# Kernel optimization log

Hardware: AMD Instinct MI355X
Metric: run time of the kernel (lower is better)

## Reference

```python
import jax, jax.numpy as jnp
import numpy as np
from jax import lax

D_MODEL, D_STATE, D_CONV, EXPAND = 192, 16, 3, 2
D_INNER = EXPAND * D_MODEL          # 384
DT_RANK = -(-D_MODEL // 16)         # 12
LN_EPS = 1e-5


def setup_inputs() -> dict:
    key = jax.random.key(0)
    ks = jax.random.split(key, 12)
    B, H, W = 4, 64, 64
    inv_sq = lambda n: 1.0 / np.sqrt(n)
    x = jax.random.normal(ks[0], (B, H, W, D_MODEL), jnp.float32)
    prompt = jax.random.normal(ks[1], (B, H, W, D_MODEL), jnp.float32)
    W_in = jax.random.normal(ks[2], (D_MODEL, 2 * D_INNER), jnp.float32) * inv_sq(D_MODEL)
    conv_w = jax.random.normal(ks[3], (D_INNER, 1, D_CONV, D_CONV), jnp.float32) * inv_sq(D_CONV * D_CONV)
    conv_b = jax.random.normal(ks[4], (D_INNER,), jnp.float32) * 0.02
    Wx = jax.random.normal(ks[5], (D_INNER, DT_RANK + 2 * D_STATE), jnp.float32) * inv_sq(D_INNER)
    Wdt = jax.random.uniform(ks[6], (DT_RANK, D_INNER), jnp.float32, -DT_RANK ** -0.5, DT_RANK ** -0.5)
    # dt bias init: inverse softplus of dt ~ LogUniform(1e-3, 0.1)
    dt = jnp.exp(jax.random.uniform(ks[7], (D_INNER,), jnp.float32) * (np.log(0.1) - np.log(1e-3)) + np.log(1e-3))
    dt = jnp.clip(dt, 1e-4, None)
    b_dt = dt + jnp.log(-jnp.expm1(-dt))
    A_log = jnp.log(jnp.broadcast_to(jnp.arange(1, D_STATE + 1, dtype=jnp.float32), (D_INNER, D_STATE)))
    D = jnp.ones((D_INNER,), jnp.float32)
    Wp = jax.random.normal(ks[8], (D_MODEL, D_STATE), jnp.float32) * inv_sq(D_MODEL)
    ln_g = jnp.ones((D_INNER,), jnp.float32)
    ln_b = jnp.zeros((D_INNER,), jnp.float32)
    Wout = jax.random.normal(ks[9], (D_INNER, D_MODEL), jnp.float32) * inv_sq(D_INNER)
    return dict(x=x, prompt=prompt, W_in=W_in, conv_w=conv_w, conv_b=conv_b, Wx=Wx,
                Wdt=Wdt, b_dt=b_dt, A_log=A_log, D=D, Wp=Wp, ln_g=ln_g, ln_b=ln_b, Wout=Wout)


def _selective_scan(u, delta, A, Bs, Cs, D):
    # u, delta: [B, L, d]; Bs, Cs: [B, L, n]; A: [d, n]; D: [d]
    Bsz = u.shape[0]
    h0 = jnp.zeros((Bsz, D_INNER, D_STATE), u.dtype)

    def step(h, inp):
        dl, uu, b, c = inp                      # [B,d],[B,d],[B,n],[B,n]
        dA = jnp.exp(dl[..., None] * A)          # [B,d,n]
        h = dA * h + (dl * uu)[..., None] * b[:, None, :]
        y = jnp.einsum('bdn,bn->bd', h, c)
        return h, y

    xs = (jnp.moveaxis(delta, 1, 0), jnp.moveaxis(u, 1, 0),
          jnp.moveaxis(Bs, 1, 0), jnp.moveaxis(Cs, 1, 0))
    _, ys = lax.scan(step, h0, xs)               # ys: [L,B,d]
    return jnp.moveaxis(ys, 0, 1) + u * D        # [B,L,d]


def reference(x, prompt, W_in, conv_w, conv_b, Wx, Wdt, b_dt, A_log, D, Wp, ln_g, ln_b, Wout):
    B, H, W, C = x.shape
    L = H * W
    xz = x @ W_in                                 # [B,H,W,2*d_inner]
    xi, z = jnp.split(xz, 2, axis=-1)
    # depthwise conv2d (NCHW, groups=d_inner)
    xc = jnp.transpose(xi, (0, 3, 1, 2))
    pad = (D_CONV - 1) // 2
    xc = lax.conv_general_dilated(xc, conv_w, (1, 1), [(pad, pad), (pad, pad)],
                                  dimension_numbers=('NCHW', 'OIHW', 'NCHW'),
                                  feature_group_count=D_INNER)
    xc = xc + conv_b[None, :, None, None]
    xc = jax.nn.silu(xc)
    u = jnp.transpose(xc.reshape(B, D_INNER, L), (0, 2, 1))   # [B,L,d]
    x_dbl = u @ Wx                                            # [B,L,r+2n]
    dtr = x_dbl[..., :DT_RANK]
    Bs = x_dbl[..., DT_RANK:DT_RANK + D_STATE]
    Cs = x_dbl[..., DT_RANK + D_STATE:]
    delta = jax.nn.softplus(dtr @ Wdt + b_dt)                 # [B,L,d] (delta_bias + softplus)
    Cs = Cs + prompt.reshape(B, L, C) @ Wp                    # prompt-conditioned C
    A = -jnp.exp(A_log)                                       # [d,n]
    y = _selective_scan(u, delta, A, Bs, Cs, D)               # [B,L,d]
    # out_norm (LayerNorm over d_inner)
    mu = jnp.mean(y, axis=-1, keepdims=True)
    var = jnp.mean(jnp.square(y - mu), axis=-1, keepdims=True)
    y = (y - mu) * lax.rsqrt(var + LN_EPS) * ln_g + ln_b
    y = y.reshape(B, H, W, D_INNER)
    y = y * jax.nn.silu(z)
    return y @ Wout
```

## Files before the change

### kernel.cpp

```cpp
#include <hip/hip_runtime.h>
#include <hip/hip_bf16.h>

#define BB 4
#define HH 64
#define WW 64
#define LL 4096
#define DM 192
#define DI 384
#define NS 16
#define RK 12
#define NC 256
#define CH 16
#define ROWS 16384
#define XDS 64
#define KA 576
#define LOG2E 1.44269504f
#define LN2   0.69314718f

typedef __bf16 bf16x8 __attribute__((ext_vector_type(8)));
typedef float  f32x4  __attribute__((ext_vector_type(4)));

#if defined(__has_builtin)
#if __has_builtin(__builtin_amdgcn_exp2f)
#define fexp2(x) __builtin_amdgcn_exp2f(x)
#else
#define fexp2(x) exp2f(x)
#endif
#else
#define fexp2(x) exp2f(x)
#endif

__device__ __forceinline__ float fsilu(float x) {
    return x / (1.0f + __expf(-x));
}

__device__ __forceinline__ unsigned short f2bf(float f) {
    unsigned int u = __float_as_uint(f);
    unsigned int r = (u + 0x7fffu + ((u >> 16) & 1u)) >> 16;
    return (unsigned short)r;
}
__device__ __forceinline__ float bf2f(unsigned short v) {
    return __uint_as_float((unsigned int)v << 16);
}

__global__ __launch_bounds__(256) void f32_to_bf16_vec(
    const float* __restrict__ src, unsigned short* __restrict__ dst, int n4)
{
    int i = blockIdx.x * 256 + threadIdx.x;
    if (i < n4) {
        float4 v = ((const float4*)src)[i];
        ((ushort4*)dst)[i] = make_ushort4(f2bf(v.x), f2bf(v.y), f2bf(v.z), f2bf(v.w));
    }
}

__global__ __launch_bounds__(256) void prompt_to_across(
    const float* __restrict__ prompt, unsigned short* __restrict__ Across)
{
    int i4 = blockIdx.x * 256 + threadIdx.x;
    if (i4 >= ROWS * (DM / 4)) return;
    int row = i4 / (DM / 4), c4 = i4 % (DM / 4);
    float4 v = ((const float4*)prompt)[i4];
    *(ushort4*)&Across[(size_t)row * KA + DI + c4 * 4] =
        make_ushort4(f2bf(v.x), f2bf(v.y), f2bf(v.z), f2bf(v.w));
}

__global__ __launch_bounds__(256) void build_bt(
    const float* __restrict__ src, unsigned short* __restrict__ dst,
    int K, int Nsrc, int Nrows)
{
    int idx = blockIdx.x * 256 + threadIdx.x;
    if (idx >= Nrows * K) return;
    int n = idx / K, k = idx % K;
    dst[idx] = (n < Nsrc) ? f2bf(src[k * Nsrc + n]) : (unsigned short)0;
}

__global__ __launch_bounds__(256) void build_bxt(
    const float* __restrict__ Wx, const float* __restrict__ Wp,
    unsigned short* __restrict__ dst)
{
    int idx = blockIdx.x * 256 + threadIdx.x;
    if (idx >= XDS * KA) return;
    int n = idx / KA, k = idx % KA;
    float v = 0.f;
    if (k < DI) { if (n < 44) v = Wx[k * 44 + n]; }
    else        { if (n >= 28 && n < 44) v = Wp[(k - DI) * NS + (n - 28)]; }
    dst[idx] = f2bf(v);
}

template<bool SPLIT>
__global__ __launch_bounds__(256) void gemm_bf16_mfma(
    const unsigned short* __restrict__ A, const unsigned short* __restrict__ BT,
    float* __restrict__ C0, unsigned short* __restrict__ C1z,
    int M, int N, int K, int halfN)
{
    __shared__ __align__(16) char lds[64 * 80 * 2];
    char* As = lds;
    char* Bs = lds + 64 * 80;
    const int tid = threadIdx.x;
    const int w = tid >> 6, lane = tid & 63;
    const int wm = w >> 1, wn = w & 1;
    const int row0 = blockIdx.x * 64, col0 = blockIdx.y * 64;
    const int r = tid >> 2, cch = tid & 3;
    const int l15 = lane & 15, k8 = lane >> 4;

    f32x4 acc[2][2] = {};
    for (int k0 = 0; k0 < K; k0 += 32) {
        *(float4*)(As + r * 80 + cch * 16) =
            *(const float4*)(A + (size_t)(row0 + r) * K + k0 + cch * 8);
        *(float4*)(Bs + r * 80 + cch * 16) =
            *(const float4*)(BT + (size_t)(col0 + r) * K + k0 + cch * 8);
        __syncthreads();
        bf16x8 a0 = *(const bf16x8*)(As + (wm * 32 +      l15) * 80 + k8 * 16);
        bf16x8 a1 = *(const bf16x8*)(As + (wm * 32 + 16 + l15) * 80 + k8 * 16);
        bf16x8 b0 = *(const bf16x8*)(Bs + (wn * 32 +      l15) * 80 + k8 * 16);
        bf16x8 b1 = *(const bf16x8*)(Bs + (wn * 32 + 16 + l15) * 80 + k8 * 16);
        acc[0][0] = __builtin_amdgcn_mfma_f32_16x16x32_bf16(a0, b0, acc[0][0], 0, 0, 0);
        acc[0][1] = __builtin_amdgcn_mfma_f32_16x16x32_bf16(a0, b1, acc[0][1], 0, 0, 0);
        acc[1][0] = __builtin_amdgcn_mfma_f32_16x16x32_bf16(a1, b0, acc[1][0], 0, 0, 0);
        acc[1][1] = __builtin_amdgcn_mfma_f32_16x16x32_bf16(a1, b1, acc[1][1], 0, 0, 0);
        __syncthreads();
    }

    if (SPLIT && col0 >= halfN) {
        const int cbase = col0 - halfN;
        #pragma unroll
        for (int fm = 0; fm < 2; ++fm)
            #pragma unroll
            for (int fn = 0; fn < 2; ++fn)
                #pragma unroll
                for (int reg = 0; reg < 4; ++reg) {
                    int row = row0 + wm * 32 + fm * 16 + k8 * 4 + reg;
                    int col = cbase + wn * 32 + fn * 16 + l15;
                    C1z[(size_t)row * halfN + col] = f2bf(acc[fm][fn][reg]);
                }
    } else {
        const int cstride = SPLIT ? halfN : N;
        #pragma unroll
        for (int fm = 0; fm < 2; ++fm)
            #pragma unroll
            for (int fn = 0; fn < 2; ++fn)
                #pragma unroll
                for (int reg = 0; reg < 4; ++reg) {
                    int row = row0 + wm * 32 + fm * 16 + k8 * 4 + reg;
                    int col = col0 + wn * 32 + fn * 16 + l15;
                    C0[(size_t)row * cstride + col] = acc[fm][fn][reg];
                }
    }
}

__global__ __launch_bounds__(256) void conv_dw_silu(
    const float* __restrict__ xi, const float* __restrict__ conv_w,
    const float* __restrict__ conv_b, unsigned short* __restrict__ Across)
{
    int idx = blockIdx.x * 256 + threadIdx.x;
    int c4 = idx % 96;
    int rest = idx / 96;
    int w = rest % WW; rest /= WW;
    int h = rest % HH;
    int b = rest / HH;
    int c = c4 * 4;

    float wgt[4][9];
    #pragma unroll
    for (int q = 0; q < 4; ++q)
        #pragma unroll
        for (int t = 0; t < 9; ++t)
            wgt[q][t] = conv_w[(c + q) * 9 + t];

    float4 acc = *(const float4*)&conv_b[c];
    #pragma unroll
    for (int kh = 0; kh < 3; ++kh) {
        int hh = h + kh - 1;
        if ((unsigned)hh >= HH) continue;
        #pragma unroll
        for (int kw = 0; kw < 3; ++kw) {
            int ww = w + kw - 1;
            if ((unsigned)ww >= WW) continue;
            const float4 xv = *(const float4*)&xi[(((size_t)(b * HH + hh)) * WW + ww) * DI + c];
            int t = kh * 3 + kw;
            acc.x += xv.x * wgt[0][t];
            acc.y += xv.y * wgt[1][t];
            acc.z += xv.z * wgt[2][t];
            acc.w += xv.w * wgt[3][t];
        }
    }
    acc.x = fsilu(acc.x); acc.y = fsilu(acc.y);
    acc.z = fsilu(acc.z); acc.w = fsilu(acc.w);
    size_t off = (((size_t)b * LL) + h * WW + w) * KA + c;
    *(ushort4*)&Across[off] = make_ushort4(f2bf(acc.x), f2bf(acc.y), f2bf(acc.z), f2bf(acc.w));
}

__global__ __launch_bounds__(256) void scan_p1_v5(
    const unsigned short* __restrict__ uA, const float* __restrict__ xdbl,
    const float* __restrict__ A_log, const float* __restrict__ Wdt,
    const float* __restrict__ b_dt, float* __restrict__ AH)
{
    const int g = blockIdx.x * 256 + threadIdx.x;
    const int d = g % DI;
    const int bc = g / DI;
    const int b = bc / NC, c = bc % NC;

    float Adn[NS], h[NS];
    {
        const float4* ap4 = (const float4*)(A_log + d * NS);
        #pragma unroll
        for (int q = 0; q < 4; ++q) {
            const float4 v = ap4[q];
            Adn[q*4+0] = -__expf(v.x) * LOG2E;
            Adn[q*4+1] = -__expf(v.y) * LOG2E;
            Adn[q*4+2] = -__expf(v.z) * LOG2E;
            Adn[q*4+3] = -__expf(v.w) * LOG2E;
        }
    }
    float wdt[RK];
    #pragma unroll
    for (int r = 0; r < RK; ++r) wdt[r] = Wdt[r * DI + d];
    const float bdt = b_dt[d];
    #pragma unroll
    for (int n = 0; n < NS; ++n) h[n] = 0.f;

    const size_t rbase = (size_t)(b * LL + c * CH);
    const unsigned short* up = uA + rbase * KA + d;
    const float* xp = xdbl + rbase * XDS;

    float uu = bf2f(up[0]);
    float4 bb0 = *(const float4*)(xp + 12), bb1 = *(const float4*)(xp + 16);
    float4 bb2 = *(const float4*)(xp + 20), bb3 = *(const float4*)(xp + 24);
    float sdlt = 0.f;

    for (int i = 0; i < CH; ++i) {
        const float* xr = xp + (size_t)i * XDS;
        const float4 t0 = *(const float4*)(xr + 0);
        const float4 t1 = *(const float4*)(xr + 4);
        const float4 t2 = *(const float4*)(xr + 8);
        const float uu_n = bf2f(up[(size_t)(i + 1) * KA]);
        const float* xn = xp + (size_t)(i + 1) * XDS;
        const float4 bn0 = *(const float4*)(xn + 12), bn1 = *(const float4*)(xn + 16);
        const float4 bn2 = *(const float4*)(xn + 20), bn3 = *(const float4*)(xn + 24);

        float t = bdt;
        t += t0.x * wdt[0] + t0.y * wdt[1] + t0.z * wdt[2]  + t0.w * wdt[3];
        t += t1.x * wdt[4] + t1.y * wdt[5] + t1.z * wdt[6]  + t1.w * wdt[7];
        t += t2.x * wdt[8] + t2.y * wdt[9] + t2.z * wdt[10] + t2.w * wdt[11];
        const float dlt = (t > 20.f) ? t : LN2 * __log2f(1.f + fexp2(t * LOG2E));

        const float du = dlt * uu;
        sdlt += dlt;
        const float bs[NS] = {bb0.x, bb0.y, bb0.z, bb0.w, bb1.x, bb1.y, bb1.z, bb1.w,
                              bb2.x, bb2.y, bb2.z, bb2.w, bb3.x, bb3.y, bb3.z, bb3.w};
        #pragma unroll
        for (int n = 0; n < NS; ++n) {
            const float a = fexp2(dlt * Adn[n]);
            h[n] = a * h[n] + du * bs[n];
        }
        uu = uu_n;
        bb0 = bn0; bb1 = bn1; bb2 = bn2; bb3 = bn3;
    }
    float* dst = AH + 2 * (((size_t)bc * DI + d) * NS);
    #pragma unroll
    for (int q = 0; q < 8; ++q) {
        const float ap0 = fexp2(sdlt * Adn[2*q]);
        const float ap1 = fexp2(sdlt * Adn[2*q+1]);
        *(float4*)(dst + 4 * q) = make_float4(ap0, h[2*q], ap1, h[2*q+1]);
    }
}

__global__ __launch_bounds__(256) void scan_p2(float2* __restrict__ AH)
{
    const int gid = blockIdx.x * 256 + threadIdx.x;
    const int dn = gid % (DI * NS);
    const int b  = gid / (DI * NS);
    const size_t base = (size_t)b * NC * DI * NS + dn;
    const size_t cs = (size_t)DI * NS;

    float2 buf[4];
    #pragma unroll
    for (int k = 0; k < 4; ++k) buf[k] = AH[base + (size_t)k * cs];

    float hin = 0.f;
    for (int c = 0; c < NC; c += 4) {
        #pragma unroll
        for (int k = 0; k < 4; ++k) {
            const int cn = (c + k + 4 < NC) ? (c + k + 4) : (NC - 1);
            const float2 nxt = AH[base + (size_t)cn * cs];
            const float2 cur = buf[k];
            AH[base + (size_t)(c + k) * cs].x = hin;
            hin = cur.x * hin + cur.y;
            buf[k] = nxt;
        }
    }
}

__global__ __launch_bounds__(384) void scan_p3_ln_v3(
    const unsigned short* __restrict__ uA, const unsigned short* __restrict__ z_bf,
    const float* __restrict__ xdbl, const float* __restrict__ AH,
    const float* __restrict__ A_log, const float* __restrict__ Wdt,
    const float* __restrict__ b_dt, const float* __restrict__ Dvec,
    const float* __restrict__ ln_g, const float* __restrict__ ln_b,
    unsigned short* __restrict__ yin_bf)
{
    __shared__ float red_s[2][8], red_sq[2][8];
    const int d = threadIdx.x;
    const int bc = blockIdx.x;
    const int b = bc / NC, c = bc % NC;
    const int wid = d >> 6, lane = d & 63;

    float Adn[NS], h[NS];
    {
        const float4* ap4 = (const float4*)(A_log + d * NS);
        #pragma unroll
        for (int q = 0; q < 4; ++q) {
            const float4 v = ap4[q];
            Adn[q*4+0] = -__expf(v.x) * LOG2E;
            Adn[q*4+1] = -__expf(v.y) * LOG2E;
            Adn[q*4+2] = -__expf(v.z) * LOG2E;
            Adn[q*4+3] = -__expf(v.w) * LOG2E;
        }
    }
    float wdt[RK];
    #pragma unroll
    for (int r = 0; r < RK; ++r) wdt[r] = Wdt[r * DI + d];
    const float bdt = b_dt[d];
    {
        const float* hp = AH + 2 * (((size_t)bc * DI + d) * NS);
        #pragma unroll
        for (int q = 0; q < 8; ++q) {
            const float4 v = *(const float4*)(hp + 4 * q);
            h[2*q] = v.x; h[2*q+1] = v.z;
        }
    }
    const float Dd = Dvec[d];
    const float lg = ln_g[d], lb = ln_b[d];

    const size_t rbase = (size_t)(b * LL + c * CH);
    const unsigned short* up = uA + rbase * KA + d;
    const unsigned short* zp = z_bf + rbase * DI + d;
    const float* xp = xdbl + rbase * XDS;
    unsigned short* yp = yin_bf + rbase * DI + d;

    float uu = bf2f(up[0]), zz = bf2f(zp[0]);
    float4 bb0 = *(const float4*)(xp + 12), bb1 = *(const float4*)(xp + 16);
    float4 bb2 = *(const float4*)(xp + 20), bb3 = *(const float4*)(xp + 24);
    float4 cc0 = *(const float4*)(xp + 28), cc1 = *(const float4*)(xp + 32);
    float4 cc2 = *(const float4*)(xp + 36), cc3 = *(const float4*)(xp + 40);

    for (int i = 0; i < CH; ++i) {
        const float* xr = xp + (size_t)i * XDS;
        const float4 t0 = *(const float4*)(xr + 0);
        const float4 t1 = *(const float4*)(xr + 4);
        const float4 t2 = *(const float4*)(xr + 8);
        const float uu_n = bf2f(up[(size_t)(i + 1) * KA]);
        const float zz_n = bf2f(zp[(size_t)(i + 1) * DI]);
        const float* xn = xp + (size_t)(i + 1) * XDS;
        const float4 bn0 = *(const float4*)(xn + 12), bn1 = *(const float4*)(xn + 16);
        const float4 bn2 = *(const float4*)(xn + 20), bn3 = *(const float4*)(xn + 24);
        const float4 cn0 = *(const float4*)(xn + 28), cn1 = *(const float4*)(xn + 32);
        const float4 cn2 = *(const float4*)(xn + 36), cn3 = *(const float4*)(xn + 40);

        float t = bdt;
        t += t0.x * wdt[0] + t0.y * wdt[1] + t0.z * wdt[2]  + t0.w * wdt[3];
        t += t1.x * wdt[4] + t1.y * wdt[5] + t1.z * wdt[6]  + t1.w * wdt[7];
        t += t2.x * wdt[8] + t2.y * wdt[9] + t2.z * wdt[10] + t2.w * wdt[11];
        const float dlt = (t > 20.f) ? t : LN2 * __log2f(1.f + fexp2(t * LOG2E));

        const float du = dlt * uu;
        const float bs[NS] = {bb0.x, bb0.y, bb0.z, bb0.w, bb1.x, bb1.y, bb1.z, bb1.w,
                              bb2.x, bb2.y, bb2.z, bb2.w, bb3.x, bb3.y, bb3.z, bb3.w};
        const float cs[NS] = {cc0.x, cc0.y, cc0.z, cc0.w, cc1.x, cc1.y, cc1.z, cc1.w,
                              cc2.x, cc2.y, cc2.z, cc2.w, cc3.x, cc3.y, cc3.z, cc3.w};
        float acc = uu * Dd;
        #pragma unroll
        for (int n = 0; n < NS; ++n) {
            const float a = fexp2(dlt * Adn[n]);
            h[n] = a * h[n] + du * bs[n];
            acc += h[n] * cs[n];
        }
        float s = acc, sq = acc * acc;
        #pragma unroll
        for (int m = 1; m < 64; m <<= 1) {
            s  += __shfl_xor(s, m);
            sq += __shfl_xor(sq, m);
        }
        const int par = i & 1;
        if (lane == 0) { red_s[par][wid] = s; red_sq[par][wid] = sq; }
        __syncthreads();
        s = red_s[par][0] + red_s[par][1] + red_s[par][2]
          + red_s[par][3] + red_s[par][4] + red_s[par][5];
        sq = red_sq[par][0] + red_sq[par][1] + red_sq[par][2]
           + red_sq[par][3] + red_sq[par][4] + red_sq[par][5];
        const float mu = s * (1.f / DI);
        const float var = sq * (1.f / DI) - mu * mu;
        const float inv = rsqrtf(var + 1e-5f);
        const float yn = (acc - mu) * inv * lg + lb;
        yp[(size_t)i * DI] = f2bf(yn * fsilu(zz));

        uu = uu_n; zz = zz_n;
        bb0 = bn0; bb1 = bn1; bb2 = bn2; bb3 = bn3;
        cc0 = cn0; cc1 = cn1; cc2 = cn2; cc3 = cn3;
    }
}

extern "C" void kernel_launch(void* const* d_in, const int* in_sizes, int n_in,
                              void* d_out, int out_size, void* d_ws, size_t ws_size,
                              hipStream_t stream)
{
    const float* x      = (const float*)d_in[0];
    const float* prompt = (const float*)d_in[1];
    const float* W_in   = (const float*)d_in[2];
    const float* conv_w = (const float*)d_in[3];
    const float* conv_b = (const float*)d_in[4];
    const float* Wx     = (const float*)d_in[5];
    const float* Wdt    = (const float*)d_in[6];
    const float* b_dt   = (const float*)d_in[7];
    const float* A_log  = (const float*)d_in[8];
    const float* Dvec   = (const float*)d_in[9];
    const float* Wp     = (const float*)d_in[10];
    const float* ln_g   = (const float*)d_in[11];
    const float* ln_b   = (const float*)d_in[12];
    const float* Wout   = (const float*)d_in[13];
    float* out = (float*)d_out;

    char* p = (char*)d_ws;
    float* xi = (float*)p;                 p += (size_t)ROWS * DI * 4;
    unsigned short* z_bf = (unsigned short*)p;  p += (size_t)(ROWS + 1) * DI * 2;
    unsigned short* Across = (unsigned short*)p; p += (size_t)(ROWS + 1) * KA * 2;
    float* xdbl = (float*)p;               p += (size_t)(ROWS + 1) * XDS * 4;
    char* ahreg = p;
    float* AH = (float*)p;                 p += (size_t)BB * NC * DI * NS * 8;
    unsigned short* WinT  = (unsigned short*)p;  p += (size_t)(2 * DI) * DM * 2;
    unsigned short* BxT   = (unsigned short*)p;  p += (size_t)XDS * KA * 2;
    unsigned short* WoutT = (unsigned short*)p;  p += (size_t)DM * DI * 2;
    unsigned short* x_bf = (unsigned short*)ahreg;
    unsigned short* yin_bf = (unsigned short*)xi;

    f32_to_bf16_vec<<<(ROWS * DM / 4 + 255) / 256, 256, 0, stream>>>(x, x_bf, ROWS * DM / 4);
    prompt_to_across<<<(ROWS * (DM / 4) + 255) / 256, 256, 0, stream>>>(prompt, Across);
    build_bt<<<(2 * DI * DM + 255) / 256, 256, 0, stream>>>(W_in, WinT, DM, 2 * DI, 2 * DI);
    build_bxt<<<(XDS * KA + 255) / 256, 256, 0, stream>>>(Wx, Wp, BxT);
    build_bt<<<(DM * DI + 255) / 256, 256, 0, stream>>>(Wout, WoutT, DI, DM, DM);

    {
        dim3 g(ROWS / 64, (2 * DI) / 64);
        gemm_bf16_mfma<true><<<g, 256, 0, stream>>>(x_bf, WinT, xi, z_bf, ROWS, 2 * DI, DM, DI);
    }
    conv_dw_silu<<<(BB * HH * WW * 96) / 256, 256, 0, stream>>>(xi, conv_w, conv_b, Across);
    {
        dim3 g(ROWS / 64, 1);
        gemm_bf16_mfma<false><<<g, 256, 0, stream>>>(Across, BxT, xdbl, nullptr, ROWS, XDS, KA, 0);
    }
    scan_p1_v5<<<(BB * NC * DI) / 256, 256, 0, stream>>>(Across, xdbl, A_log, Wdt, b_dt, AH);
    scan_p2<<<(BB * DI * NS) / 256, 256, 0, stream>>>((float2*)AH);
    scan_p3_ln_v3<<<BB * NC, 384, 0, stream>>>(Across, z_bf, xdbl, AH, A_log, Wdt,
                                               b_dt, Dvec, ln_g, ln_b, yin_bf);
    {
        dim3 g(ROWS / 64, DM / 64);
        gemm_bf16_mfma<false><<<g, 256, 0, stream>>>(yin_bf, WoutT, out, nullptr, ROWS, DM, DI, 0);
    }
}
```

Before: 279.3 us.

## Stage xdbl chunk in LDS, preload u/z, batch LayerNorm reductions in scan

Both chunked scan kernels now use one block per (batch, chunk) with 384 threads. The block cooperatively copies the chunk's xdbl rows into shared memory, so the broadcast B/C/dt reads come from LDS instead of repeated global loads. All 16 u (and z) values are preloaded into registers up front. In the output kernel, the per-timestep __syncthreads for the LayerNorm reduction is replaced by per-step partial sums into a CH-sized shared array, with a single barrier and a normalization pass afterwards. This trades higher register pressure (accs, uu, zz arrays) and possible occupancy loss for fewer barriers and fewer global loads.

```diff
diff --git a/kernel.cpp b/kernel.cpp
--- a/kernel.cpp
+++ b/kernel.cpp
@@ -190,15 +190,19 @@
     *(ushort4*)&Across[off] = make_ushort4(f2bf(acc.x), f2bf(acc.y), f2bf(acc.z), f2bf(acc.w));
 }
 
-__global__ __launch_bounds__(256) void scan_p1_v5(
+__global__ __launch_bounds__(384) void scan_p1_v6(
     const unsigned short* __restrict__ uA, const float* __restrict__ xdbl,
     const float* __restrict__ A_log, const float* __restrict__ Wdt,
     const float* __restrict__ b_dt, float* __restrict__ AH)
 {
-    const int g = blockIdx.x * 256 + threadIdx.x;
-    const int d = g % DI;
-    const int bc = g / DI;
+    __shared__ __align__(16) float xlds[CH * XDS];
+    const int d = threadIdx.x;
+    const int bc = blockIdx.x;
     const int b = bc / NC, c = bc % NC;
+    const size_t rbase = (size_t)(b * LL + c * CH);
+
+    for (int i = d; i < CH * XDS; i += 384)
+        xlds[i] = xdbl[rbase * XDS + i];
 
     float Adn[NS], h[NS];
     {
@@ -219,32 +223,29 @@
     #pragma unroll
     for (int n = 0; n < NS; ++n) h[n] = 0.f;
 
-    const size_t rbase = (size_t)(b * LL + c * CH);
-    const unsigned short* up = uA + rbase * KA + d;
-    const float* xp = xdbl + rbase * XDS;
-
-    float uu = bf2f(up[0]);
-    float4 bb0 = *(const float4*)(xp + 12), bb1 = *(const float4*)(xp + 16);
-    float4 bb2 = *(const float4*)(xp + 20), bb3 = *(const float4*)(xp + 24);
+    float uu[CH];
+    {
+        const unsigned short* up = uA + rbase * KA + d;
+        #pragma unroll
+        for (int i = 0; i < CH; ++i) uu[i] = bf2f(up[(size_t)i * KA]);
+    }
+    __syncthreads();
+
     float sdlt = 0.f;
-
+    #pragma unroll
     for (int i = 0; i < CH; ++i) {
-        const float* xr = xp + (size_t)i * XDS;
+        const float* xr = xlds + i * XDS;
         const float4 t0 = *(const float4*)(xr + 0);
         const float4 t1 = *(const float4*)(xr + 4);
         const float4 t2 = *(const float4*)(xr + 8);
-        const float uu_n = bf2f(up[(size_t)(i + 1) * KA]);
-        const float* xn = xp + (size_t)(i + 1) * XDS;
-        const float4 bn0 = *(const float4*)(xn + 12), bn1 = *(const float4*)(xn + 16);
-        const float4 bn2 = *(const float4*)(xn + 20), bn3 = *(const float4*)(xn + 24);
-
+        const float4 bb0 = *(const float4*)(xr + 12), bb1 = *(const float4*)(xr + 16);
+        const float4 bb2 = *(const float4*)(xr + 20), bb3 = *(const float4*)(xr + 24);
         float t = bdt;
         t += t0.x * wdt[0] + t0.y * wdt[1] + t0.z * wdt[2]  + t0.w * wdt[3];
         t += t1.x * wdt[4] + t1.y * wdt[5] + t1.z * wdt[6]  + t1.w * wdt[7];
         t += t2.x * wdt[8] + t2.y * wdt[9] + t2.z * wdt[10] + t2.w * wdt[11];
         const float dlt = (t > 20.f) ? t : LN2 * __log2f(1.f + fexp2(t * LOG2E));
-
-        const float du = dlt * uu;
+        const float du = dlt * uu[i];
         sdlt += dlt;
         const float bs[NS] = {bb0.x, bb0.y, bb0.z, bb0.w, bb1.x, bb1.y, bb1.z, bb1.w,
                               bb2.x, bb2.y, bb2.z, bb2.w, bb3.x, bb3.y, bb3.z, bb3.w};
@@ -253,8 +254,6 @@
             const float a = fexp2(dlt * Adn[n]);
             h[n] = a * h[n] + du * bs[n];
         }
-        uu = uu_n;
-        bb0 = bn0; bb1 = bn1; bb2 = bn2; bb3 = bn3;
     }
     float* dst = AH + 2 * (((size_t)bc * DI + d) * NS);
     #pragma unroll
@@ -291,7 +290,7 @@
     }
 }
 
-__global__ __launch_bounds__(384) void scan_p3_ln_v3(
+__global__ __launch_bounds__(384) void scan_p3_ln_v4(
     const unsigned short* __restrict__ uA, const unsigned short* __restrict__ z_bf,
     const float* __restrict__ xdbl, const float* __restrict__ AH,
     const float* __restrict__ A_log, const float* __restrict__ Wdt,
@@ -299,11 +298,16 @@
     const float* __restrict__ ln_g, const float* __restrict__ ln_b,
     unsigned short* __restrict__ yin_bf)
 {
-    __shared__ float red_s[2][8], red_sq[2][8];
+    __shared__ __align__(16) float xlds[CH * XDS];
+    __shared__ float red_s[CH][8], red_sq[CH][8];
     const int d = threadIdx.x;
     const int bc = blockIdx.x;
     const int b = bc / NC, c = bc % NC;
     const int wid = d >> 6, lane = d & 63;
+    const size_t rbase = (size_t)(b * LL + c * CH);
+
+    for (int i = d; i < CH * XDS; i += 384)
+        xlds[i] = xdbl[rbase * XDS + i];
 
     float Adn[NS], h[NS];
     {
@@ -332,71 +336,70 @@
     const float Dd = Dvec[d];
     const float lg = ln_g[d], lb = ln_b[d];
 
-    const size_t rbase = (size_t)(b * LL + c * CH);
-    const unsigned short* up = uA + rbase * KA + d;
-    const unsigned short* zp = z_bf + rbase * DI + d;
-    const float* xp = xdbl + rbase * XDS;
-    unsigned short* yp = yin_bf + rbase * DI + d;
-
-    float uu = bf2f(up[0]), zz = bf2f(zp[0]);
-    float4 bb0 = *(const float4*)(xp + 12), bb1 = *(const float4*)(xp + 16);
-    float4 bb2 = *(const float4*)(xp + 20), bb3 = *(const float4*)(xp + 24);
-    float4 cc0 = *(const float4*)(xp + 28), cc1 = *(const float4*)(xp + 32);
-    float4 cc2 = *(const float4*)(xp + 36), cc3 = *(const float4*)(xp + 40);
-
+    float uu[CH], zz[CH];
+    {
+        const unsigned short* up = uA + rbase * KA + d;
+        const unsigned short* zp = z_bf + rbase * DI + d;
+        #pragma unroll
+        for (int i = 0; i < CH; ++i) {
+            uu[i] = bf2f(up[(size_t)i * KA]);
+            zz[i] = bf2f(zp[(size_t)i * DI]);
+        }
+    }
+    __syncthreads();
+
+    float accs[CH];
+    #pragma unroll
     for (int i = 0; i < CH; ++i) {
-        const float* xr = xp + (size_t)i * XDS;
+        const float* xr = xlds + i * XDS;
         const float4 t0 = *(const float4*)(xr + 0);
         const float4 t1 = *(const float4*)(xr + 4);
         const float4 t2 = *(const float4*)(xr + 8);
-        const float uu_n = bf2f(up[(size_t)(i + 1) * KA]);
-        const float zz_n = bf2f(zp[(size_t)(i + 1) * DI]);
-        const float* xn = xp + (size_t)(i + 1) * XDS;
-        const float4 bn0 = *(const float4*)(xn + 12), bn1 = *(const float4*)(xn + 16);
-        const float4 bn2 = *(const float4*)(xn + 20), bn3 = *(const float4*)(xn + 24);
-        const float4 cn0 = *(const float4*)(xn + 28), cn1 = *(const float4*)(xn + 32);
-        const float4 cn2 = *(const float4*)(xn + 36), cn3 = *(const float4*)(xn + 40);
-
+        const float4 bb0 = *(const float4*)(xr + 12), bb1 = *(const float4*)(xr + 16);
+        const float4 bb2 = *(const float4*)(xr + 20), bb3 = *(const float4*)(xr + 24);
+        const float4 cc0 = *(const float4*)(xr + 28), cc1 = *(const float4*)(xr + 32);
+        const float4 cc2 = *(const float4*)(xr + 36), cc3 = *(const float4*)(xr + 40);
         float t = bdt;
         t += t0.x * wdt[0] + t0.y * wdt[1] + t0.z * wdt[2]  + t0.w * wdt[3];
         t += t1.x * wdt[4] + t1.y * wdt[5] + t1.z * wdt[6]  + t1.w * wdt[7];
         t += t2.x * wdt[8] + t2.y * wdt[9] + t2.z * wdt[10] + t2.w * wdt[11];
         const float dlt = (t > 20.f) ? t : LN2 * __log2f(1.f + fexp2(t * LOG2E));
-
-        const float du = dlt * uu;
+        const float du = dlt * uu[i];
         const float bs[NS] = {bb0.x, bb0.y, bb0.z, bb0.w, bb1.x, bb1.y, bb1.z, bb1.w,
                               bb2.x, bb2.y, bb2.z, bb2.w, bb3.x, bb3.y, bb3.z, bb3.w};
         const float cs[NS] = {cc0.x, cc0.y, cc0.z, cc0.w, cc1.x, cc1.y, cc1.z, cc1.w,
                               cc2.x, cc2.y, cc2.z, cc2.w, cc3.x, cc3.y, cc3.z, cc3.w};
-        float acc = uu * Dd;
+        float acc = uu[i] * Dd;
         #pragma unroll
         for (int n = 0; n < NS; ++n) {
             const float a = fexp2(dlt * Adn[n]);
             h[n] = a * h[n] + du * bs[n];
             acc += h[n] * cs[n];
         }
+        accs[i] = acc;
         float s = acc, sq = acc * acc;
         #pragma unroll
         for (int m = 1; m < 64; m <<= 1) {
             s  += __shfl_xor(s, m);
             sq += __shfl_xor(sq, m);
         }
-        const int par = i & 1;
-        if (lane == 0) { red_s[par][wid] = s; red_sq[par][wid] = sq; }
-        __syncthreads();
-        s = red_s[par][0] + red_s[par][1] + red_s[par][2]
-          + red_s[par][3] + red_s[par][4] + red_s[par][5];
-        sq = red_sq[par][0] + red_sq[par][1] + red_sq[par][2]
-           + red_sq[par][3] + red_sq[par][4] + red_sq[par][5];
+        if (lane == 0) { red_s[i][wid] = s; red_sq[i][wid] = sq; }
+    }
+
+    __syncthreads();
+
+    unsigned short* yp = yin_bf + rbase * DI + d;
+    #pragma unroll
+    for (int i = 0; i < CH; ++i) {
+        const float s = red_s[i][0] + red_s[i][1] + red_s[i][2]
+                      + red_s[i][3] + red_s[i][4] + red_s[i][5];
+        const float sq = red_sq[i][0] + red_sq[i][1] + red_sq[i][2]
+                       + red_sq[i][3] + red_sq[i][4] + red_sq[i][5];
         const float mu = s * (1.f / DI);
         const float var = sq * (1.f / DI) - mu * mu;
         const float inv = rsqrtf(var + 1e-5f);
-        const float yn = (acc - mu) * inv * lg + lb;
-        yp[(size_t)i * DI] = f2bf(yn * fsilu(zz));
-
-        uu = uu_n; zz = zz_n;
-        bb0 = bn0; bb1 = bn1; bb2 = bn2; bb3 = bn3;
-        cc0 = cn0; cc1 = cn1; cc2 = cn2; cc3 = cn3;
+        const float yn = (accs[i] - mu) * inv * lg + lb;
+        yp[(size_t)i * DI] = f2bf(yn * fsilu(zz[i]));
     }
 }
 
@@ -448,9 +451,9 @@
         dim3 g(ROWS / 64, 1);
         gemm_bf16_mfma<false><<<g, 256, 0, stream>>>(Across, BxT, xdbl, nullptr, ROWS, XDS, KA, 0);
     }
-    scan_p1_v5<<<(BB * NC * DI) / 256, 256, 0, stream>>>(Across, xdbl, A_log, Wdt, b_dt, AH);
+    scan_p1_v6<<<BB * NC, 384, 0, stream>>>(Across, xdbl, A_log, Wdt, b_dt, AH);
     scan_p2<<<(BB * DI * NS) / 256, 256, 0, stream>>>((float2*)AH);
-    scan_p3_ln_v3<<<BB * NC, 384, 0, stream>>>(Across, z_bf, xdbl, AH, A_log, Wdt,
+    scan_p3_ln_v4<<<BB * NC, 384, 0, stream>>>(Across, z_bf, xdbl, AH, A_log, Wdt,
                                                b_dt, Dvec, ln_g, ln_b, yin_bf);
     {
         dim3 g(ROWS / 64, DM / 64);
```

New measurement: 289.6 us. 1.04x slower.

## Stage xdbl chunks in LDS for scan phases and write compact carry-in buffer

Applied to the files above, without the earlier changes.

Scan phase 1 and phase 3 now copy each chunk's 16x64 xdbl rows into shared memory once per block and read the dt, B and C values from LDS. Before this, every thread issued redundant global float4 loads, even though those values are identical across the 384 channels. Phase 1 now uses one block per chunk with 384 threads and fully unrolls its time loop. Phase 2 writes the carry-in state to a separate dense float buffer instead of overwriting fields inside the interleaved AH array, so phase 3 reads half the bytes using contiguous float4 loads. The trade-offs are an extra workspace allocation, a barrier, and more register pressure from the unrolled loops.

```diff
diff --git a/kernel.cpp b/kernel.cpp
--- a/kernel.cpp
+++ b/kernel.cpp
@@ -190,15 +190,19 @@
     *(ushort4*)&Across[off] = make_ushort4(f2bf(acc.x), f2bf(acc.y), f2bf(acc.z), f2bf(acc.w));
 }
 
-__global__ __launch_bounds__(256) void scan_p1_v5(
+__global__ __launch_bounds__(384) void scan_p1_v7(
     const unsigned short* __restrict__ uA, const float* __restrict__ xdbl,
     const float* __restrict__ A_log, const float* __restrict__ Wdt,
     const float* __restrict__ b_dt, float* __restrict__ AH)
 {
-    const int g = blockIdx.x * 256 + threadIdx.x;
-    const int d = g % DI;
-    const int bc = g / DI;
+    __shared__ __align__(16) float xlds[CH * XDS];
+    const int d = threadIdx.x;
+    const int bc = blockIdx.x;
     const int b = bc / NC, c = bc % NC;
+    const size_t rbase = (size_t)(b * LL + c * CH);
+
+    for (int i = d; i < CH * XDS; i += 384)
+        xlds[i] = xdbl[rbase * XDS + i];
 
     float Adn[NS], h[NS];
     {
@@ -219,31 +223,25 @@
     #pragma unroll
     for (int n = 0; n < NS; ++n) h[n] = 0.f;
 
-    const size_t rbase = (size_t)(b * LL + c * CH);
     const unsigned short* up = uA + rbase * KA + d;
-    const float* xp = xdbl + rbase * XDS;
-
     float uu = bf2f(up[0]);
-    float4 bb0 = *(const float4*)(xp + 12), bb1 = *(const float4*)(xp + 16);
-    float4 bb2 = *(const float4*)(xp + 20), bb3 = *(const float4*)(xp + 24);
+    __syncthreads();
+
     float sdlt = 0.f;
-
+    #pragma unroll
     for (int i = 0; i < CH; ++i) {
-        const float* xr = xp + (size_t)i * XDS;
+        const float uu_n = bf2f(up[(size_t)(i + 1) * KA]);
+        const float* xr = xlds + i * XDS;
         const float4 t0 = *(const float4*)(xr + 0);
         const float4 t1 = *(const float4*)(xr + 4);
         const float4 t2 = *(const float4*)(xr + 8);
-        const float uu_n = bf2f(up[(size_t)(i + 1) * KA]);
-        const float* xn = xp + (size_t)(i + 1) * XDS;
-        const float4 bn0 = *(const float4*)(xn + 12), bn1 = *(const float4*)(xn + 16);
-        const float4 bn2 = *(const float4*)(xn + 20), bn3 = *(const float4*)(xn + 24);
-
+        const float4 bb0 = *(const float4*)(xr + 12), bb1 = *(const float4*)(xr + 16);
+        const float4 bb2 = *(const float4*)(xr + 20), bb3 = *(const float4*)(xr + 24);
         float t = bdt;
         t += t0.x * wdt[0] + t0.y * wdt[1] + t0.z * wdt[2]  + t0.w * wdt[3];
         t += t1.x * wdt[4] + t1.y * wdt[5] + t1.z * wdt[6]  + t1.w * wdt[7];
         t += t2.x * wdt[8] + t2.y * wdt[9] + t2.z * wdt[10] + t2.w * wdt[11];
         const float dlt = (t > 20.f) ? t : LN2 * __log2f(1.f + fexp2(t * LOG2E));
-
         const float du = dlt * uu;
         sdlt += dlt;
         const float bs[NS] = {bb0.x, bb0.y, bb0.z, bb0.w, bb1.x, bb1.y, bb1.z, bb1.w,
@@ -254,7 +252,6 @@
             h[n] = a * h[n] + du * bs[n];
         }
         uu = uu_n;
-        bb0 = bn0; bb1 = bn1; bb2 = bn2; bb3 = bn3;
     }
     float* dst = AH + 2 * (((size_t)bc * DI + d) * NS);
     #pragma unroll
@@ -265,7 +262,8 @@
     }
 }
 
-__global__ __launch_bounds__(256) void scan_p2(float2* __restrict__ AH)
+__global__ __launch_bounds__(256) void scan_p2_v2(
+    const float2* __restrict__ AH, float* __restrict__ Hinc)
 {
     const int gid = blockIdx.x * 256 + threadIdx.x;
     const int dn = gid % (DI * NS);
@@ -284,26 +282,31 @@
             const int cn = (c + k + 4 < NC) ? (c + k + 4) : (NC - 1);
             const float2 nxt = AH[base + (size_t)cn * cs];
             const float2 cur = buf[k];
-            AH[base + (size_t)(c + k) * cs].x = hin;
+            Hinc[base + (size_t)(c + k) * cs] = hin;
             hin = cur.x * hin + cur.y;
             buf[k] = nxt;
         }
     }
 }
 
-__global__ __launch_bounds__(384) void scan_p3_ln_v3(
+__global__ __launch_bounds__(384) void scan_p3_ln_v5(
     const unsigned short* __restrict__ uA, const unsigned short* __restrict__ z_bf,
-    const float* __restrict__ xdbl, const float* __restrict__ AH,
+    const float* __restrict__ xdbl, const float* __restrict__ Hinc,
     const float* __restrict__ A_log, const float* __restrict__ Wdt,
     const float* __restrict__ b_dt, const float* __restrict__ Dvec,
     const float* __restrict__ ln_g, const float* __restrict__ ln_b,
     unsigned short* __restrict__ yin_bf)
 {
+    __shared__ __align__(16) float xlds[CH * XDS];
     __shared__ float red_s[2][8], red_sq[2][8];
     const int d = threadIdx.x;
     const int bc = blockIdx.x;
     const int b = bc / NC, c = bc % NC;
     const int wid = d >> 6, lane = d & 63;
+    const size_t rbase = (size_t)(b * LL + c * CH);
+
+    for (int i = d; i < CH * XDS; i += 384)
+        xlds[i] = xdbl[rbase * XDS + i];
 
     float Adn[NS], h[NS];
     {
@@ -322,47 +325,40 @@
     for (int r = 0; r < RK; ++r) wdt[r] = Wdt[r * DI + d];
     const float bdt = b_dt[d];
     {
-        const float* hp = AH + 2 * (((size_t)bc * DI + d) * NS);
-        #pragma unroll
-        for (int q = 0; q < 8; ++q) {
+        const float* hp = Hinc + ((size_t)bc * DI + d) * NS;
+        #pragma unroll
+        for (int q = 0; q < 4; ++q) {
             const float4 v = *(const float4*)(hp + 4 * q);
-            h[2*q] = v.x; h[2*q+1] = v.z;
+            h[q*4] = v.x; h[q*4+1] = v.y; h[q*4+2] = v.z; h[q*4+3] = v.w;
         }
     }
     const float Dd = Dvec[d];
     const float lg = ln_g[d], lb = ln_b[d];
 
-    const size_t rbase = (size_t)(b * LL + c * CH);
     const unsigned short* up = uA + rbase * KA + d;
     const unsigned short* zp = z_bf + rbase * DI + d;
-    const float* xp = xdbl + rbase * XDS;
     unsigned short* yp = yin_bf + rbase * DI + d;
 
     float uu = bf2f(up[0]), zz = bf2f(zp[0]);
-    float4 bb0 = *(const float4*)(xp + 12), bb1 = *(const float4*)(xp + 16);
-    float4 bb2 = *(const float4*)(xp + 20), bb3 = *(const float4*)(xp + 24);
-    float4 cc0 = *(const float4*)(xp + 28), cc1 = *(const float4*)(xp + 32);
-    float4 cc2 = *(const float4*)(xp + 36), cc3 = *(const float4*)(xp + 40);
-
+    __syncthreads();
+
+    #pragma unroll
     for (int i = 0; i < CH; ++i) {
-        const float* xr = xp + (size_t)i * XDS;
+        const float uu_n = bf2f(up[(size_t)(i + 1) * KA]);
+        const float zz_n = bf2f(zp[(size_t)(i + 1) * DI]);
+        const float* xr = xlds + i * XDS;
         const float4 t0 = *(const float4*)(xr + 0);
         const float4 t1 = *(const float4*)(xr + 4);
         const float4 t2 = *(const float4*)(xr + 8);
-        const float uu_n = bf2f(up[(size_t)(i + 1) * KA]);
-        const float zz_n = bf2f(zp[(size_t)(i + 1) * DI]);
-        const float* xn = xp + (size_t)(i + 1) * XDS;
-        const float4 bn0 = *(const float4*)(xn + 12), bn1 = *(const float4*)(xn + 16);
-        const float4 bn2 = *(const float4*)(xn + 20), bn3 = *(const float4*)(xn + 24);
-        const float4 cn0 = *(const float4*)(xn + 28), cn1 = *(const float4*)(xn + 32);
-        const float4 cn2 = *(const float4*)(xn + 36), cn3 = *(const float4*)(xn + 40);
-
+        const float4 bb0 = *(const float4*)(xr + 12), bb1 = *(const float4*)(xr + 16);
+        const float4 bb2 = *(const float4*)(xr + 20), bb3 = *(const float4*)(xr + 24);
+        const float4 cc0 = *(const float4*)(xr + 28), cc1 = *(const float4*)(xr + 32);
+        const float4 cc2 = *(const float4*)(xr + 36), cc3 = *(const float4*)(xr + 40);
         float t = bdt;
         t += t0.x * wdt[0] + t0.y * wdt[1] + t0.z * wdt[2]  + t0.w * wdt[3];
         t += t1.x * wdt[4] + t1.y * wdt[5] + t1.z * wdt[6]  + t1.w * wdt[7];
         t += t2.x * wdt[8] + t2.y * wdt[9] + t2.z * wdt[10] + t2.w * wdt[11];
         const float dlt = (t > 20.f) ? t : LN2 * __log2f(1.f + fexp2(t * LOG2E));
-
         const float du = dlt * uu;
         const float bs[NS] = {bb0.x, bb0.y, bb0.z, bb0.w, bb1.x, bb1.y, bb1.z, bb1.w,
                               bb2.x, bb2.y, bb2.z, bb2.w, bb3.x, bb3.y, bb3.z, bb3.w};
@@ -395,8 +391,6 @@
         yp[(size_t)i * DI] = f2bf(yn * fsilu(zz));
 
         uu = uu_n; zz = zz_n;
-        bb0 = bn0; bb1 = bn1; bb2 = bn2; bb3 = bn3;
-        cc0 = cn0; cc1 = cn1; cc2 = cn2; cc3 = cn3;
     }
 }
 
@@ -427,6 +421,7 @@
     float* xdbl = (float*)p;               p += (size_t)(ROWS + 1) * XDS * 4;
     char* ahreg = p;
     float* AH = (float*)p;                 p += (size_t)BB * NC * DI * NS * 8;
+    float* Hinc = (float*)p;               p += (size_t)BB * NC * DI * NS * 4;
     unsigned short* WinT  = (unsigned short*)p;  p += (size_t)(2 * DI) * DM * 2;
     unsigned short* BxT   = (unsigned short*)p;  p += (size_t)XDS * KA * 2;
     unsigned short* WoutT = (unsigned short*)p;  p += (size_t)DM * DI * 2;
@@ -448,9 +443,9 @@
         dim3 g(ROWS / 64, 1);
         gemm_bf16_mfma<false><<<g, 256, 0, stream>>>(Across, BxT, xdbl, nullptr, ROWS, XDS, KA, 0);
     }
-    scan_p1_v5<<<(BB * NC * DI) / 256, 256, 0, stream>>>(Across, xdbl, A_log, Wdt, b_dt, AH);
-    scan_p2<<<(BB * DI * NS) / 256, 256, 0, stream>>>((float2*)AH);
-    scan_p3_ln_v3<<<BB * NC, 384, 0, stream>>>(Across, z_bf, xdbl, AH, A_log, Wdt,
+    scan_p1_v7<<<BB * NC, 384, 0, stream>>>(Across, xdbl, A_log, Wdt, b_dt, AH);
+    scan_p2_v2<<<(BB * DI * NS) / 256, 256, 0, stream>>>((const float2*)AH, Hinc);
+    scan_p3_ln_v5<<<BB * NC, 384, 0, stream>>>(Across, z_bf, xdbl, Hinc, A_log, Wdt,
                                                b_dt, Dvec, ln_g, ln_b, yin_bf);
     {
         dim3 g(ROWS / 64, DM / 64);
```

Measured after the change: 288.4 us. 3.3% more time.
